# Kernel optimization log

Measured on AMD Instinct MI355X. Metric: run time of the kernel, lower is better.

The kernel has to match this reference:

```python
import jax, jax.numpy as jnp
import numpy as np

NU, NI, D, E = 200_000, 100_000, 128, 600_000
EPS = 1e-5


def _linear(x, W, b):
    # torch nn.Linear: y = x @ W.T + b, W is [out, in]
    return x @ W.T + b


def _layer_norm(x, g, b):
    mu = jnp.mean(x, axis=-1, keepdims=True)
    var = jnp.mean((x - mu) ** 2, axis=-1, keepdims=True)
    return (x - mu) * jax.lax.rsqrt(var + EPS) * g + b


def _sym_norm_w(row, col, n_src, n_dst):
    ones = jnp.ones(row.shape, jnp.float32)
    deg_s = jax.ops.segment_sum(ones, row, num_segments=n_src)
    deg_d = jax.ops.segment_sum(ones, col, num_segments=n_dst)
    inv_s = jnp.where(deg_s > 0, deg_s ** -0.5, 0.0)
    inv_d = jnp.where(deg_d > 0, deg_d ** -0.5, 0.0)
    return inv_s[row] * inv_d[col]  # [E]


def _relation(x_src, row, col, n_dst, Wl, bl, Wf, bf):
    w = _sym_norm_w(row, col, x_src.shape[0], n_dst)
    m = x_src[row] * w[:, None]                      # gather + scale, [E, D]
    s = jax.ops.segment_sum(m, col, num_segments=n_dst)      # sum messages
    sq = jax.ops.segment_sum(m * m, col, num_segments=n_dst)  # sum of squares
    fm = 0.5 * (s * s - sq)                          # FM interaction
    return _linear(s, Wl, bl) + _linear(fm, Wf, bf)


def setup_inputs() -> dict:
    key = jax.random.key(0)
    ks = jax.random.split(key, 24)
    scale = 1.0 / np.sqrt(D)
    p = lambda k: jax.random.normal(k, (D, D), jnp.float32) * scale
    return {
        "h_user": jax.random.normal(ks[0], (NU, D), jnp.float32),
        "h_item": jax.random.normal(ks[1], (NI, D), jnp.float32),
        "ei_u2i_src": jax.random.randint(ks[2], (E,), 0, NU),
        "ei_u2i_dst": jax.random.randint(ks[3], (E,), 0, NI),
        "ei_i2u_src": jax.random.randint(ks[4], (E,), 0, NI),
        "ei_i2u_dst": jax.random.randint(ks[5], (E,), 0, NU),
        "Ws_user": p(ks[6]), "bs_user": jnp.zeros((D,), jnp.float32),
        "Ws_item": p(ks[7]), "bs_item": jnp.zeros((D,), jnp.float32),
        "Wlin_u2i": p(ks[8]), "blin_u2i": jnp.zeros((D,), jnp.float32),
        "Wfm_u2i": p(ks[9]), "bfm_u2i": jnp.zeros((D,), jnp.float32),
        "Wlin_i2u": p(ks[10]), "blin_i2u": jnp.zeros((D,), jnp.float32),
        "Wfm_i2u": p(ks[11]), "bfm_i2u": jnp.zeros((D,), jnp.float32),
        "g_user": jnp.ones((D,), jnp.float32), "be_user": jnp.zeros((D,), jnp.float32),
        "g_item": jnp.ones((D,), jnp.float32), "be_item": jnp.zeros((D,), jnp.float32),
    }


def reference(h_user, h_item, ei_u2i_src, ei_u2i_dst, ei_i2u_src, ei_i2u_dst,
              Ws_user, bs_user, Ws_item, bs_item,
              Wlin_u2i, blin_u2i, Wfm_u2i, bfm_u2i,
              Wlin_i2u, blin_i2u, Wfm_i2u, bfm_i2u,
              g_user, be_user, g_item, be_item):
    out_u = _linear(h_user, Ws_user, bs_user)
    out_i = _linear(h_item, Ws_item, bs_item)
    # edge type (user, rates, item): src=user, dst=item
    out_i = out_i + _relation(h_user, ei_u2i_src, ei_u2i_dst, NI,
                              Wlin_u2i, blin_u2i, Wfm_u2i, bfm_u2i)
    # edge type (item, rated_by, user): src=item, dst=user
    out_u = out_u + _relation(h_item, ei_i2u_src, ei_i2u_dst, NU,
                              Wlin_i2u, blin_i2u, Wfm_i2u, bfm_i2u)
    out_u = jax.nn.relu(_layer_norm(out_u, g_user, be_user))
    out_i = jax.nn.relu(_layer_norm(out_i, g_item, be_item))
    return out_u, out_i
```

## Files before the change

### kernel.cpp

```cpp
#include <hip/hip_runtime.h>
#include <hip/hip_bf16.h>

#define NU 200000
#define NI 100000
#define DD 128
#define EE 600000
#define CAP 28
#define ZN4 ((2 * NU + 2 * NI) / 4)
#define ZB  ((ZN4 + 255) / 256)
#define NW8 (6 * DD * DD / 8)
#define NWB ((NW8 + 255) / 256)
#define NPB2 ((2 * EE + 255) / 256)
#define NIV ((NU + NI + 255) / 256)
#define NGAB ((NI + 3) / 4)
#define NGBB ((NU + 3) / 4)
#define NMA ((NI + 127) / 128)
#define NMB ((NU + 127) / 128)

typedef __attribute__((ext_vector_type(8))) short bf16x8;
typedef __attribute__((ext_vector_type(4))) float f32x4;

__device__ __forceinline__ unsigned short f2bf(float f) {
    unsigned int u = __float_as_uint(f);
    u += 0x7fff + ((u >> 16) & 1);
    return (unsigned short)(u >> 16);
}

__global__ void prep_kernel(int* __restrict__ z,
                            const float* __restrict__ w0, const float* __restrict__ w1,
                            const float* __restrict__ w2, const float* __restrict__ w3,
                            const float* __restrict__ w4, const float* __restrict__ w5,
                            unsigned short* __restrict__ wb) {
    int b = blockIdx.x;
    if (b < ZB) {
        int i = b * 256 + threadIdx.x;
        if (i < ZN4) ((int4*)z)[i] = make_int4(0, 0, 0, 0);
        return;
    }
    int i = (b - ZB) * 256 + threadIdx.x;
    if (i >= NW8) return;
    int wsel = i >> 11;
    int k = i & 2047;
    const float* src = (wsel == 0) ? w0 : (wsel == 1) ? w1 : (wsel == 2) ? w2
                     : (wsel == 3) ? w3 : (wsel == 4) ? w4 : w5;
    const float4* p = (const float4*)src + (size_t)k * 2;
    float4 v0 = p[0], v1 = p[1];
    union { unsigned short us[8]; uint4 u4; } r;
    r.us[0] = f2bf(v0.x); r.us[1] = f2bf(v0.y); r.us[2] = f2bf(v0.z); r.us[3] = f2bf(v0.w);
    r.us[4] = f2bf(v1.x); r.us[5] = f2bf(v1.y); r.us[6] = f2bf(v1.z); r.us[7] = f2bf(v1.w);
    ((uint4*)(wb + wsel * DD * DD))[k] = r.u4;
}

__global__ void place2_kernel(const int* __restrict__ srcA, const int* __restrict__ dstA,
                              const int* __restrict__ srcB, const int* __restrict__ dstB,
                              int* __restrict__ degAs, int* __restrict__ cntA, int* __restrict__ bktA,
                              int* __restrict__ degBs, int* __restrict__ cntB, int* __restrict__ bktB) {
    int e = blockIdx.x * 256 + threadIdx.x;
    if (e < EE) {
        int r = srcA[e], c = dstA[e];
        atomicAdd(&degAs[r], 1);
        int slot = atomicAdd(&cntA[c], 1);
        if (slot < CAP) bktA[c * CAP + slot] = r;
    } else if (e < 2 * EE) {
        int f = e - EE;
        int r = srcB[f], c = dstB[f];
        atomicAdd(&degBs[r], 1);
        int slot = atomicAdd(&cntB[c], 1);
        if (slot < CAP) bktB[c * CAP + slot] = r;
    }
}

__global__ void inv2_kernel(const int* __restrict__ degAs, const int* __restrict__ degBs,
                            float* __restrict__ invAs, float* __restrict__ invBs) {
    int i = blockIdx.x * 256 + threadIdx.x;
    if (i < NU) {
        int v = degAs[i];
        invAs[i] = (v > 0) ? rsqrtf((float)v) : 0.f;
    } else if (i < NU + NI) {
        int j = i - NU;
        int v = degBs[j];
        invBs[j] = (v > 0) ? rsqrtf((float)v) : 0.f;
    }
}

__device__ __forceinline__ void gather_rows(const float* __restrict__ x,
                                            const int* __restrict__ cnt,
                                            const float* __restrict__ invS,
                                            const int* __restrict__ bkt,
                                            unsigned short* __restrict__ sOut,
                                            unsigned short* __restrict__ fmOut,
                                            int N, int bid) {
    int d = bid * 4 + (threadIdx.x >> 6);
    int lane = threadIdx.x & 63;
    if (d >= N) return;
    int cfull = cnt[d];
    float invD = (cfull > 0) ? rsqrtf((float)cfull) : 0.f;
    int dg = min(cfull, CAP);
    const int* brow = bkt + (size_t)d * CAP;
    float s0 = 0.f, s1 = 0.f, q0 = 0.f, q1 = 0.f;
    for (int j = 0; j < dg; j += 4) {
        int rem = dg - j;
        int4 iv = *(const int4*)(brow + j);
        int i0 = iv.x;
        int i1 = (rem > 1) ? iv.y : i0;
        int i2 = (rem > 2) ? iv.z : i0;
        int i3 = (rem > 3) ? iv.w : i0;
        float w0 = invS[i0] * invD;
        float w1 = (rem > 1) ? invS[i1] * invD : 0.f;
        float w2 = (rem > 2) ? invS[i2] * invD : 0.f;
        float w3 = (rem > 3) ? invS[i3] * invD : 0.f;
        float2 v0 = *(const float2*)(x + (size_t)i0 * DD + lane * 2);
        float2 v1 = *(const float2*)(x + (size_t)i1 * DD + lane * 2);
        float2 v2 = *(const float2*)(x + (size_t)i2 * DD + lane * 2);
        float2 v3 = *(const float2*)(x + (size_t)i3 * DD + lane * 2);
        float a, b;
        a = v0.x * w0; b = v0.y * w0; s0 += a; q0 += a * a; s1 += b; q1 += b * b;
        a = v1.x * w1; b = v1.y * w1; s0 += a; q0 += a * a; s1 += b; q1 += b * b;
        a = v2.x * w2; b = v2.y * w2; s0 += a; q0 += a * a; s1 += b; q1 += b * b;
        a = v3.x * w3; b = v3.y * w3; s0 += a; q0 += a * a; s1 += b; q1 += b * b;
    }
    float f0 = 0.5f * (s0 * s0 - q0), f1 = 0.5f * (s1 * s1 - q1);
    unsigned int spack = (unsigned int)f2bf(s0) | ((unsigned int)f2bf(s1) << 16);
    unsigned int fpack = (unsigned int)f2bf(f0) | ((unsigned int)f2bf(f1) << 16);
    *(unsigned int*)(sOut  + (size_t)d * DD + lane * 2) = spack;
    *(unsigned int*)(fmOut + (size_t)d * DD + lane * 2) = fpack;
}

__global__ __launch_bounds__(256) void gather2_kernel(
        const float* __restrict__ h_user, const float* __restrict__ h_item,
        const int* __restrict__ cntA, const float* __restrict__ invAs, const int* __restrict__ bktA,
        const int* __restrict__ cntB, const float* __restrict__ invBs, const int* __restrict__ bktB,
        unsigned short* __restrict__ sbA, unsigned short* __restrict__ fbA,
        unsigned short* __restrict__ sbB, unsigned short* __restrict__ fbB) {
    int b = blockIdx.x;
    if (b < NGAB) {
        gather_rows(h_user, cntA, invAs, bktA, sbA, fbA, NI, b);
    } else {
        gather_rows(h_item, cntB, invBs, bktB, sbB, fbB, NU, b - NGAB);
    }
}

__device__ __forceinline__ bf16x8 a_from_f32(const float* __restrict__ X, size_t off) {
    float4 lo = *(const float4*)(X + off);
    float4 hi = *(const float4*)(X + off + 4);
    union { unsigned short us[8]; bf16x8 v; } r;
    r.us[0] = f2bf(lo.x); r.us[1] = f2bf(lo.y); r.us[2] = f2bf(lo.z); r.us[3] = f2bf(lo.w);
    r.us[4] = f2bf(hi.x); r.us[5] = f2bf(hi.y); r.us[6] = f2bf(hi.z); r.us[7] = f2bf(hi.w);
    return r.v;
}

__device__ __forceinline__ void gemm_ln_block(unsigned char* Wlds, int bid,
        const float* __restrict__ Xh32,
        const unsigned short* __restrict__ Xs, const unsigned short* __restrict__ Xf,
        const unsigned short* __restrict__ W0, const unsigned short* __restrict__ W1,
        const unsigned short* __restrict__ W2,
        const float* __restrict__ B0, const float* __restrict__ B1,
        const float* __restrict__ B2,
        const float* __restrict__ g, const float* __restrict__ be,
        float* __restrict__ out, int N) {
    int tid  = threadIdx.x;
    int wv   = tid >> 6, lane = tid & 63;
    int rlo  = lane & 15, kg = lane >> 4;
    int rowbase = bid * 128 + wv * 32;
    int ar0 = min(rowbase + rlo,      N - 1);
    int ar1 = min(rowbase + 16 + rlo, N - 1);

    f32x4 acc[2][8];
    #pragma unroll
    for (int rt = 0; rt < 2; ++rt)
        #pragma unroll
        for (int jt = 0; jt < 8; ++jt) acc[rt][jt] = (f32x4){0.f, 0.f, 0.f, 0.f};

    const unsigned short* Wp[3] = {W0, W1, W2};
    size_t a0off = (size_t)ar0 * DD + kg * 8;
    size_t a1off = (size_t)ar1 * DD + kg * 8;
    #pragma unroll
    for (int s3 = 0; s3 < 3; ++s3) {
        const uint4* Wg = (const uint4*)Wp[s3];
        #pragma unroll
        for (int it = 0; it < 8; ++it) {
            int slot = it * 256 + tid;
            int row = slot >> 4, c = slot & 15;
            uint4 v = Wg[slot];
            int sc = c ^ (row & 7);
            *(uint4*)(Wlds + ((row << 8) + (sc << 4))) = v;
        }
        __syncthreads();
        #pragma unroll
        for (int ks = 0; ks < 4; ++ks) {
            bf16x8 bfr[8];
            #pragma unroll
            for (int jt = 0; jt < 8; ++jt) {
                int jrow = jt * 16 + rlo;
                int boff = (jrow << 8) + ((((ks << 2) + kg) ^ (jrow & 7)) << 4);
                bfr[jt] = *(const bf16x8*)(Wlds + boff);
            }
            bf16x8 a0, a1;
            if (s3 == 0) {
                a0 = a_from_f32(Xh32, a0off + ks * 32);
                a1 = a_from_f32(Xh32, a1off + ks * 32);
            } else {
                const unsigned short* X = (s3 == 1) ? Xs : Xf;
                a0 = *(const bf16x8*)(X + a0off + ks * 32);
                a1 = *(const bf16x8*)(X + a1off + ks * 32);
            }
            #pragma unroll
            for (int jt = 0; jt < 8; ++jt)
                acc[0][jt] = __builtin_amdgcn_mfma_f32_16x16x32_bf16(a0, bfr[jt], acc[0][jt], 0, 0, 0);
            #pragma unroll
            for (int jt = 0; jt < 8; ++jt)
                acc[1][jt] = __builtin_amdgcn_mfma_f32_16x16x32_bf16(a1, bfr[jt], acc[1][jt], 0, 0, 0);
        }
        __syncthreads();
    }

    float bsum[8], gg[8], bb[8];
    #pragma unroll
    for (int jt = 0; jt < 8; ++jt) {
        int col = jt * 16 + rlo;
        bsum[jt] = B0[col] + B1[col] + B2[col];
        gg[jt] = g[col]; bb[jt] = be[col];
    }
    #pragma unroll
    for (int rt = 0; rt < 2; ++rt) {
        float s1[4] = {0.f, 0.f, 0.f, 0.f}, s2[4] = {0.f, 0.f, 0.f, 0.f};
        #pragma unroll
        for (int jt = 0; jt < 8; ++jt)
            #pragma unroll
            for (int r = 0; r < 4; ++r) {
                float v = acc[rt][jt][r] + bsum[jt];
                acc[rt][jt][r] = v;
                s1[r] += v;
                s2[r] += v * v;
            }
        #pragma unroll
        for (int m = 1; m < 16; m <<= 1)
            #pragma unroll
            for (int r = 0; r < 4; ++r) {
                s1[r] += __shfl_xor(s1[r], m);
                s2[r] += __shfl_xor(s2[r], m);
            }
        #pragma unroll
        for (int r = 0; r < 4; ++r) {
            int grow = rowbase + rt * 16 + kg * 4 + r;
            if (grow >= N) continue;
            float mu  = s1[r] * (1.f / 128.f);
            float var = s2[r] * (1.f / 128.f) - mu * mu;
            float inv = rsqrtf(var + 1e-5f);
            #pragma unroll
            for (int jt = 0; jt < 8; ++jt) {
                int col = jt * 16 + rlo;
                float o = (acc[rt][jt][r] - mu) * inv * gg[jt] + bb[jt];
                out[(size_t)grow * DD + col] = fmaxf(o, 0.f);
            }
        }
    }
}

__global__ __launch_bounds__(256) void gemm2_kernel(
        const float* __restrict__ h_user, const float* __restrict__ h_item,
        const unsigned short* __restrict__ sbA, const unsigned short* __restrict__ fbA,
        const unsigned short* __restrict__ sbB, const unsigned short* __restrict__ fbB,
        const unsigned short* __restrict__ WsU, const unsigned short* __restrict__ WsI,
        const unsigned short* __restrict__ WlA, const unsigned short* __restrict__ WfA,
        const unsigned short* __restrict__ WlB, const unsigned short* __restrict__ WfB,
        const float* __restrict__ bs_user, const float* __restrict__ bs_item,
        const float* __restrict__ blA, const float* __restrict__ bfA,
        const float* __restrict__ blB, const float* __restrict__ bfB,
        const float* __restrict__ g_user, const float* __restrict__ be_user,
        const float* __restrict__ g_item, const float* __restrict__ be_item,
        float* __restrict__ out_u, float* __restrict__ out_i) {
    __shared__ __align__(16) unsigned char Wlds[32768];
    int b = blockIdx.x;
    if (b < NMA) {
        gemm_ln_block(Wlds, b, h_item, sbA, fbA, WsI, WlA, WfA,
                      bs_item, blA, bfA, g_item, be_item, out_i, NI);
    } else {
        gemm_ln_block(Wlds, b - NMA, h_user, sbB, fbB, WsU, WlB, WfB,
                      bs_user, blB, bfB, g_user, be_user, out_u, NU);
    }
}

extern "C" void kernel_launch(void* const* d_in, const int* in_sizes, int n_in,
                              void* d_out, int out_size, void* d_ws, size_t ws_size,
                              hipStream_t stream) {
    const float* h_user   = (const float*)d_in[0];
    const float* h_item   = (const float*)d_in[1];
    const int*   u2i_src  = (const int*)d_in[2];
    const int*   u2i_dst  = (const int*)d_in[3];
    const int*   i2u_src  = (const int*)d_in[4];
    const int*   i2u_dst  = (const int*)d_in[5];
    const float* Ws_user  = (const float*)d_in[6];
    const float* bs_user  = (const float*)d_in[7];
    const float* Ws_item  = (const float*)d_in[8];
    const float* bs_item  = (const float*)d_in[9];
    const float* Wlin_u2i = (const float*)d_in[10];
    const float* blin_u2i = (const float*)d_in[11];
    const float* Wfm_u2i  = (const float*)d_in[12];
    const float* bfm_u2i  = (const float*)d_in[13];
    const float* Wlin_i2u = (const float*)d_in[14];
    const float* blin_i2u = (const float*)d_in[15];
    const float* Wfm_i2u  = (const float*)d_in[16];
    const float* bfm_i2u  = (const float*)d_in[17];
    const float* g_user   = (const float*)d_in[18];
    const float* be_user  = (const float*)d_in[19];
    const float* g_item   = (const float*)d_in[20];
    const float* be_item  = (const float*)d_in[21];

    float* out   = (float*)d_out;
    float* out_u = out;
    float* out_i = out + (size_t)NU * DD;

    char* wsb = (char*)d_ws;
    int* degAs = (int*)wsb;       wsb += sizeof(int) * NU;
    int* degBs = (int*)wsb;       wsb += sizeof(int) * NI;
    int* cntA  = (int*)wsb;       wsb += sizeof(int) * NI;
    int* cntB  = (int*)wsb;       wsb += sizeof(int) * NU;
    float* invAs = (float*)wsb;   wsb += sizeof(float) * NU;
    float* invBs = (float*)wsb;   wsb += sizeof(float) * NI;
    int* bktA  = (int*)wsb;       wsb += sizeof(int) * (size_t)NI * CAP;
    int* bktB  = (int*)wsb;       wsb += sizeof(int) * (size_t)NU * CAP;
    unsigned short* sbA = (unsigned short*)wsb;  wsb += sizeof(short) * (size_t)NI * DD;
    unsigned short* fbA = (unsigned short*)wsb;  wsb += sizeof(short) * (size_t)NI * DD;
    unsigned short* sbB = (unsigned short*)wsb;  wsb += sizeof(short) * (size_t)NU * DD;
    unsigned short* fbB = (unsigned short*)wsb;  wsb += sizeof(short) * (size_t)NU * DD;
    unsigned short* wb  = (unsigned short*)wsb;  wsb += sizeof(short) * 6 * DD * DD;
    unsigned short* WsU = wb;
    unsigned short* WsI = wb + 1 * DD * DD;
    unsigned short* WlA = wb + 2 * DD * DD;
    unsigned short* WfA = wb + 3 * DD * DD;
    unsigned short* WlB = wb + 4 * DD * DD;
    unsigned short* WfB = wb + 5 * DD * DD;

    prep_kernel<<<ZB + NWB, 256, 0, stream>>>(
        degAs, Ws_user, Ws_item, Wlin_u2i, Wfm_u2i, Wlin_i2u, Wfm_i2u, wb);

    place2_kernel<<<NPB2, 256, 0, stream>>>(
        u2i_src, u2i_dst, i2u_src, i2u_dst,
        degAs, cntA, bktA, degBs, cntB, bktB);

    inv2_kernel<<<NIV, 256, 0, stream>>>(degAs, degBs, invAs, invBs);

    gather2_kernel<<<NGAB + NGBB, 256, 0, stream>>>(
        h_user, h_item, cntA, invAs, bktA, cntB, invBs, bktB,
        sbA, fbA, sbB, fbB);

    gemm2_kernel<<<NMA + NMB, 256, 0, stream>>>(
        h_user, h_item, sbA, fbA, sbB, fbB,
        WsU, WsI, WlA, WfA, WlB, WfB,
        bs_user, bs_item, blin_u2i, bfm_u2i, blin_i2u, bfm_i2u,
        g_user, be_user, g_item, be_item, out_u, out_i);
}
```

Measured before the change: 412.4 us.

## Pre-scale source features to bf16 and split degree atomics per XCD

Adds a pass that multiplies each source row by its inverse-sqrt source degree and stores it as bf16. The gather then reads half-width rows without per-neighbour weight loads, and applies the destination normalisation once at the end. Source-degree counting moves to per-XCD partitioned counters with workgroup-scope atomics, which a new kernel sums, to reduce cross-die atomic contention. This costs an extra full pass over the features and some precision, and the workgroup-scope atomics rely on same-XCD coherence.

```diff
diff --git a/kernel.cpp b/kernel.cpp
--- a/kernel.cpp
+++ b/kernel.cpp
@@ -6,12 +6,15 @@
 #define DD 128
 #define EE 600000
 #define CAP 28
-#define ZN4 ((2 * NU + 2 * NI) / 4)
+#define NXCD 8
+#define ZINT (NI + NU + NXCD * NU + NXCD * NI)
+#define ZN4 (ZINT / 4)
 #define ZB  ((ZN4 + 255) / 256)
 #define NW8 (6 * DD * DD / 8)
 #define NWB ((NW8 + 255) / 256)
 #define NPB2 ((2 * EE + 255) / 256)
 #define NIV ((NU + NI + 255) / 256)
+#define NSC (((NU + NI) * 16 + 255) / 256)
 #define NGAB ((NI + 3) / 4)
 #define NGBB ((NU + 3) / 4)
 #define NMA ((NI + 127) / 128)
@@ -24,6 +27,17 @@
     unsigned int u = __float_as_uint(f);
     u += 0x7fff + ((u >> 16) & 1);
     return (unsigned short)(u >> 16);
+}
+__device__ __forceinline__ float bf2f(unsigned short h) {
+    return __uint_as_float(((unsigned int)h) << 16);
+}
+__device__ __forceinline__ int xcc_id() {
+    unsigned x;
+    asm volatile("s_getreg_b32 %0, hwreg(HW_REG_XCC_ID)" : "=s"(x));
+    return (int)(x & 7);
+}
+__device__ __forceinline__ void atomic_inc_l2(int* p) {
+    __hip_atomic_fetch_add(p, 1, __ATOMIC_RELAXED, __HIP_MEMORY_SCOPE_WORKGROUP);
 }
 
 __global__ void prep_kernel(int* __restrict__ z,
@@ -51,41 +65,73 @@
     ((uint4*)(wb + wsel * DD * DD))[k] = r.u4;
 }
 
-__global__ void place2_kernel(const int* __restrict__ srcA, const int* __restrict__ dstA,
-                              const int* __restrict__ srcB, const int* __restrict__ dstB,
-                              int* __restrict__ degAs, int* __restrict__ cntA, int* __restrict__ bktA,
-                              int* __restrict__ degBs, int* __restrict__ cntB, int* __restrict__ bktB) {
+__global__ __launch_bounds__(256) void place2_kernel(
+        const int* __restrict__ srcA, const int* __restrict__ dstA,
+        const int* __restrict__ srcB, const int* __restrict__ dstB,
+        int* __restrict__ degAs_p, int* __restrict__ cntA, int* __restrict__ bktA,
+        int* __restrict__ degBs_p, int* __restrict__ cntB, int* __restrict__ bktB) {
     int e = blockIdx.x * 256 + threadIdx.x;
+    if (e >= 2 * EE) return;
+    int xcc = xcc_id();
     if (e < EE) {
         int r = srcA[e], c = dstA[e];
-        atomicAdd(&degAs[r], 1);
+        atomic_inc_l2(&degAs_p[xcc * NU + r]);
         int slot = atomicAdd(&cntA[c], 1);
         if (slot < CAP) bktA[c * CAP + slot] = r;
-    } else if (e < 2 * EE) {
+    } else {
         int f = e - EE;
         int r = srcB[f], c = dstB[f];
-        atomicAdd(&degBs[r], 1);
+        atomic_inc_l2(&degBs_p[xcc * NI + r]);
         int slot = atomicAdd(&cntB[c], 1);
         if (slot < CAP) bktB[c * CAP + slot] = r;
     }
 }
 
-__global__ void inv2_kernel(const int* __restrict__ degAs, const int* __restrict__ degBs,
-                            float* __restrict__ invAs, float* __restrict__ invBs) {
+__global__ void invmerge_kernel(const int* __restrict__ degAs_p,
+                                const int* __restrict__ degBs_p,
+                                float* __restrict__ invAs, float* __restrict__ invBs) {
     int i = blockIdx.x * 256 + threadIdx.x;
     if (i < NU) {
-        int v = degAs[i];
-        invAs[i] = (v > 0) ? rsqrtf((float)v) : 0.f;
+        int d = 0;
+        #pragma unroll
+        for (int x = 0; x < NXCD; ++x) d += degAs_p[x * NU + i];
+        invAs[i] = (d > 0) ? rsqrtf((float)d) : 0.f;
     } else if (i < NU + NI) {
         int j = i - NU;
-        int v = degBs[j];
-        invBs[j] = (v > 0) ? rsqrtf((float)v) : 0.f;
-    }
-}
-
-__device__ __forceinline__ void gather_rows(const float* __restrict__ x,
+        int d = 0;
+        #pragma unroll
+        for (int x = 0; x < NXCD; ++x) d += degBs_p[x * NI + j];
+        invBs[j] = (d > 0) ? rsqrtf((float)d) : 0.f;
+    }
+}
+
+__global__ void scaleconv_kernel(const float* __restrict__ h_user,
+                                 const float* __restrict__ h_item,
+                                 const float* __restrict__ invAs,
+                                 const float* __restrict__ invBs,
+                                 unsigned short* __restrict__ hubS,
+                                 unsigned short* __restrict__ hibS) {
+    int i = blockIdx.x * 256 + threadIdx.x;
+    const float* h; const float* inv; unsigned short* out; int row, k8;
+    if (i < NU * 16) { h = h_user; inv = invAs; out = hubS; row = i >> 4; k8 = (i & 15) * 8; }
+    else {
+        int j = i - NU * 16;
+        if (j >= NI * 16) return;
+        h = h_item; inv = invBs; out = hibS; row = j >> 4; k8 = (j & 15) * 8;
+    }
+    float w = inv[row];
+    const float4* p = (const float4*)(h + (size_t)row * DD + k8);
+    float4 v0 = p[0], v1 = p[1];
+    union { unsigned short us[8]; uint4 u4; } r;
+    r.us[0] = f2bf(v0.x * w); r.us[1] = f2bf(v0.y * w);
+    r.us[2] = f2bf(v0.z * w); r.us[3] = f2bf(v0.w * w);
+    r.us[4] = f2bf(v1.x * w); r.us[5] = f2bf(v1.y * w);
+    r.us[6] = f2bf(v1.z * w); r.us[7] = f2bf(v1.w * w);
+    *(uint4*)(out + (size_t)row * DD + k8) = r.u4;
+}
+
+__device__ __forceinline__ void gather_rows(const unsigned short* __restrict__ xS,
                                             const int* __restrict__ cnt,
-                                            const float* __restrict__ invS,
                                             const int* __restrict__ bkt,
                                             unsigned short* __restrict__ sOut,
                                             unsigned short* __restrict__ fmOut,
@@ -95,6 +141,7 @@
     if (d >= N) return;
     int cfull = cnt[d];
     float invD = (cfull > 0) ? rsqrtf((float)cfull) : 0.f;
+    float invD2 = invD * invD;
     int dg = min(cfull, CAP);
     const int* brow = bkt + (size_t)d * CAP;
     float s0 = 0.f, s1 = 0.f, q0 = 0.f, q1 = 0.f;
@@ -105,38 +152,43 @@
         int i1 = (rem > 1) ? iv.y : i0;
         int i2 = (rem > 2) ? iv.z : i0;
         int i3 = (rem > 3) ? iv.w : i0;
-        float w0 = invS[i0] * invD;
-        float w1 = (rem > 1) ? invS[i1] * invD : 0.f;
-        float w2 = (rem > 2) ? invS[i2] * invD : 0.f;
-        float w3 = (rem > 3) ? invS[i3] * invD : 0.f;
-        float2 v0 = *(const float2*)(x + (size_t)i0 * DD + lane * 2);
-        float2 v1 = *(const float2*)(x + (size_t)i1 * DD + lane * 2);
-        float2 v2 = *(const float2*)(x + (size_t)i2 * DD + lane * 2);
-        float2 v3 = *(const float2*)(x + (size_t)i3 * DD + lane * 2);
+        unsigned int u0 = *(const unsigned int*)(xS + (size_t)i0 * DD + lane * 2);
+        unsigned int u1 = *(const unsigned int*)(xS + (size_t)i1 * DD + lane * 2);
+        unsigned int u2 = *(const unsigned int*)(xS + (size_t)i2 * DD + lane * 2);
+        unsigned int u3 = *(const unsigned int*)(xS + (size_t)i3 * DD + lane * 2);
+        u1 = (rem > 1) ? u1 : 0u;
+        u2 = (rem > 2) ? u2 : 0u;
+        u3 = (rem > 3) ? u3 : 0u;
         float a, b;
-        a = v0.x * w0; b = v0.y * w0; s0 += a; q0 += a * a; s1 += b; q1 += b * b;
-        a = v1.x * w1; b = v1.y * w1; s0 += a; q0 += a * a; s1 += b; q1 += b * b;
-        a = v2.x * w2; b = v2.y * w2; s0 += a; q0 += a * a; s1 += b; q1 += b * b;
-        a = v3.x * w3; b = v3.y * w3; s0 += a; q0 += a * a; s1 += b; q1 += b * b;
-    }
-    float f0 = 0.5f * (s0 * s0 - q0), f1 = 0.5f * (s1 * s1 - q1);
-    unsigned int spack = (unsigned int)f2bf(s0) | ((unsigned int)f2bf(s1) << 16);
+        a = bf2f((unsigned short)(u0 & 0xffff)); b = bf2f((unsigned short)(u0 >> 16));
+        s0 += a; q0 += a * a; s1 += b; q1 += b * b;
+        a = bf2f((unsigned short)(u1 & 0xffff)); b = bf2f((unsigned short)(u1 >> 16));
+        s0 += a; q0 += a * a; s1 += b; q1 += b * b;
+        a = bf2f((unsigned short)(u2 & 0xffff)); b = bf2f((unsigned short)(u2 >> 16));
+        s0 += a; q0 += a * a; s1 += b; q1 += b * b;
+        a = bf2f((unsigned short)(u3 & 0xffff)); b = bf2f((unsigned short)(u3 >> 16));
+        s0 += a; q0 += a * a; s1 += b; q1 += b * b;
+    }
+    float ss0 = s0 * invD, ss1 = s1 * invD;
+    float f0 = 0.5f * (ss0 * ss0 - q0 * invD2);
+    float f1 = 0.5f * (ss1 * ss1 - q1 * invD2);
+    unsigned int spack = (unsigned int)f2bf(ss0) | ((unsigned int)f2bf(ss1) << 16);
     unsigned int fpack = (unsigned int)f2bf(f0) | ((unsigned int)f2bf(f1) << 16);
     *(unsigned int*)(sOut  + (size_t)d * DD + lane * 2) = spack;
     *(unsigned int*)(fmOut + (size_t)d * DD + lane * 2) = fpack;
 }
 
 __global__ __launch_bounds__(256) void gather2_kernel(
-        const float* __restrict__ h_user, const float* __restrict__ h_item,
-        const int* __restrict__ cntA, const float* __restrict__ invAs, const int* __restrict__ bktA,
-        const int* __restrict__ cntB, const float* __restrict__ invBs, const int* __restrict__ bktB,
+        const unsigned short* __restrict__ hubS, const unsigned short* __restrict__ hibS,
+        const int* __restrict__ cntA, const int* __restrict__ bktA,
+        const int* __restrict__ cntB, const int* __restrict__ bktB,
         unsigned short* __restrict__ sbA, unsigned short* __restrict__ fbA,
         unsigned short* __restrict__ sbB, unsigned short* __restrict__ fbB) {
     int b = blockIdx.x;
     if (b < NGAB) {
-        gather_rows(h_user, cntA, invAs, bktA, sbA, fbA, NI, b);
+        gather_rows(hubS, cntA, bktA, sbA, fbA, NI, b);
     } else {
-        gather_rows(h_item, cntB, invBs, bktB, sbB, fbB, NU, b - NGAB);
+        gather_rows(hibS, cntB, bktB, sbB, fbB, NU, b - NGAB);
     }
 }
 
@@ -312,14 +364,16 @@
     float* out_i = out + (size_t)NU * DD;
 
     char* wsb = (char*)d_ws;
-    int* degAs = (int*)wsb;       wsb += sizeof(int) * NU;
-    int* degBs = (int*)wsb;       wsb += sizeof(int) * NI;
-    int* cntA  = (int*)wsb;       wsb += sizeof(int) * NI;
-    int* cntB  = (int*)wsb;       wsb += sizeof(int) * NU;
+    int* cntA    = (int*)wsb;     wsb += sizeof(int) * NI;
+    int* cntB    = (int*)wsb;     wsb += sizeof(int) * NU;
+    int* degAs_p = (int*)wsb;     wsb += sizeof(int) * NXCD * NU;
+    int* degBs_p = (int*)wsb;     wsb += sizeof(int) * NXCD * NI;
     float* invAs = (float*)wsb;   wsb += sizeof(float) * NU;
     float* invBs = (float*)wsb;   wsb += sizeof(float) * NI;
     int* bktA  = (int*)wsb;       wsb += sizeof(int) * (size_t)NI * CAP;
     int* bktB  = (int*)wsb;       wsb += sizeof(int) * (size_t)NU * CAP;
+    unsigned short* hubS = (unsigned short*)wsb;  wsb += sizeof(short) * (size_t)NU * DD;
+    unsigned short* hibS = (unsigned short*)wsb;  wsb += sizeof(short) * (size_t)NI * DD;
     unsigned short* sbA = (unsigned short*)wsb;  wsb += sizeof(short) * (size_t)NI * DD;
     unsigned short* fbA = (unsigned short*)wsb;  wsb += sizeof(short) * (size_t)NI * DD;
     unsigned short* sbB = (unsigned short*)wsb;  wsb += sizeof(short) * (size_t)NU * DD;
@@ -333,17 +387,18 @@
     unsigned short* WfB = wb + 5 * DD * DD;
 
     prep_kernel<<<ZB + NWB, 256, 0, stream>>>(
-        degAs, Ws_user, Ws_item, Wlin_u2i, Wfm_u2i, Wlin_i2u, Wfm_i2u, wb);
+        cntA, Ws_user, Ws_item, Wlin_u2i, Wfm_u2i, Wlin_i2u, Wfm_i2u, wb);
 
     place2_kernel<<<NPB2, 256, 0, stream>>>(
         u2i_src, u2i_dst, i2u_src, i2u_dst,
-        degAs, cntA, bktA, degBs, cntB, bktB);
-
-    inv2_kernel<<<NIV, 256, 0, stream>>>(degAs, degBs, invAs, invBs);
+        degAs_p, cntA, bktA, degBs_p, cntB, bktB);
+
+    invmerge_kernel<<<NIV, 256, 0, stream>>>(degAs_p, degBs_p, invAs, invBs);
+
+    scaleconv_kernel<<<NSC, 256, 0, stream>>>(h_user, h_item, invAs, invBs, hubS, hibS);
 
     gather2_kernel<<<NGAB + NGBB, 256, 0, stream>>>(
-        h_user, h_item, cntA, invAs, bktA, cntB, invBs, bktB,
-        sbA, fbA, sbB, fbB);
+        hubS, hibS, cntA, bktA, cntB, bktB, sbA, fbA, sbB, fbB);
 
     gemm2_kernel<<<NMA + NMB, 256, 0, stream>>>(
         h_user, h_item, sbA, fbA, sbB, fbB,
```

After: 393.6 us. 1.05x faster.
